# Kernel optimization log

Measured on AMD Instinct MI355X. Metric: run time of the kernel, lower is better.

Reference implementation:

```python
import jax, jax.numpy as jnp
import numpy as np

B, N, D, H = 4, 1024, 1024, 16
NP = N - 1  # prototypes; +1 CLS slot -> n_valid == N
HD = D // H
LN_EPS = 1e-5


def _build_spatial_sim(key):
    centers = jax.random.uniform(key, (NP, 2), dtype=jnp.float32) * 10.0
    diff = centers[:, None, :] - centers[None, :, :]
    d2 = jnp.sum(diff * diff, axis=-1)           # squared pairwise distance
    dist = jnp.sqrt(d2)
    sigma = dist.mean()                           # spatial_sigma = mean cdist
    sim = jnp.exp(-d2 / (2.0 * sigma * sigma))
    sim = sim / sim.max()
    ext = jnp.zeros((NP + 1, NP + 1), dtype=jnp.float32)
    ext = ext.at[0, :].set(1.0).at[:, 0].set(1.0).at[1:, 1:].set(sim)
    return ext


def setup_inputs() -> dict:
    key = jax.random.key(0)
    kc, kx, kq, kp = jax.random.split(key, 4)
    spatial_sim = _build_spatial_sim(kc)          # [N, N] buffer
    x = jax.random.normal(kx, (B, N, D), dtype=jnp.float32)
    gamma = jnp.ones((D,), dtype=jnp.float32)
    beta = jnp.zeros((D,), dtype=jnp.float32)
    w_qkv = jax.random.normal(kq, (D, 3 * D), dtype=jnp.float32) * 0.02
    w_proj = jax.random.normal(kp, (D, D), dtype=jnp.float32) * 0.02
    b_proj = jnp.zeros((D,), dtype=jnp.float32)
    swl = jnp.float32(np.log(0.3 / 0.7))          # inverse_sigmoid(0.3)
    return {"x": x, "gamma": gamma, "beta": beta, "w_qkv": w_qkv,
            "w_proj": w_proj, "b_proj": b_proj,
            "spatial_weight_logit": swl, "spatial_sim": spatial_sim}


def reference(x, gamma, beta, w_qkv, w_proj, b_proj, spatial_weight_logit, spatial_sim):
    b, n, d = x.shape
    scale = HD ** (-0.5)
    # LayerNorm (biased variance, eps=1e-5)
    mu = x.mean(axis=-1, keepdims=True)
    var = jnp.mean((x - mu) ** 2, axis=-1, keepdims=True)
    x_norm = (x - mu) / jnp.sqrt(var + LN_EPS) * gamma + beta
    # QKV projection -> [B, H, N, HD] each
    qkv = (x_norm @ w_qkv).reshape(b, n, 3, H, HD)
    qkv = jnp.transpose(qkv, (2, 0, 3, 1, 4))
    q, k, v = qkv[0], qkv[1], qkv[2]
    scores = jnp.einsum('bhnd,bhmd->bhnm', q, k) * scale
    alpha = jax.nn.sigmoid(spatial_weight_logit)
    # blend feature attention with fixed spatial similarity, then softmax
    attn = jax.nn.softmax((1.0 - alpha) * scores + alpha * spatial_sim[None, None], axis=-1)
    out = jnp.einsum('bhnm,bhmd->bhnd', attn, v)
    out = jnp.transpose(out, (0, 2, 1, 3)).reshape(b, n, d)
    out = out @ w_proj + b_proj
    return x + out
```

## Files before the change

### kernel.cpp

```cpp
#include <hip/hip_runtime.h>

#define Bz 4
#define Nn 1024
#define Dd 1024
#define Hh 16
#define HD 64
#define SCALE 0.125f
#define LN_EPS 1e-5f

typedef __attribute__((ext_vector_type(8))) __bf16 bf16x8;
typedef __attribute__((ext_vector_type(4))) float f32x4;

static __device__ inline unsigned short f2bf(float f) {
    unsigned int u = __float_as_uint(f);
    u += 0x7fffu + ((u >> 16) & 1u);
    return (unsigned short)(u >> 16);
}

static __device__ inline float bf2f(unsigned short s) {
    return __uint_as_float((unsigned)s << 16);
}

static __device__ inline bf16x8 ldfrag(const unsigned short* p) {
    return *(const bf16x8*)p;
}

static __device__ __forceinline__ void glds16(const unsigned short* g, unsigned short* l) {
    __builtin_amdgcn_global_load_lds((const __attribute__((address_space(1))) void*)g,
                                     (__attribute__((address_space(3))) void*)l, 16, 0, 0);
}

__global__ __launch_bounds__(256) void ln_kernel(const float* __restrict__ x,
                                                 const float* __restrict__ gamma,
                                                 const float* __restrict__ beta,
                                                 unsigned short* __restrict__ xn) {
    int row = blockIdx.x;
    int t = threadIdx.x;
    const float* xr = x + (size_t)row * Dd;
    float4 v = ((const float4*)xr)[t];
    float s = v.x + v.y + v.z + v.w;
    float ss = v.x * v.x + v.y * v.y + v.z * v.z + v.w * v.w;
    for (int o = 32; o > 0; o >>= 1) {
        s += __shfl_down(s, o);
        ss += __shfl_down(ss, o);
    }
    __shared__ float red[8];
    int wid = t >> 6;
    if ((t & 63) == 0) { red[wid * 2] = s; red[wid * 2 + 1] = ss; }
    __syncthreads();
    float tot = red[0] + red[2] + red[4] + red[6];
    float tot2 = red[1] + red[3] + red[5] + red[7];
    float mu = tot * (1.0f / Dd);
    float var = tot2 * (1.0f / Dd) - mu * mu;
    float inv = rsqrtf(var + LN_EPS);
    float4 g = ((const float4*)gamma)[t];
    float4 b = ((const float4*)beta)[t];
    ushort4 o4;
    o4.x = f2bf((v.x - mu) * inv * g.x + b.x);
    o4.y = f2bf((v.y - mu) * inv * g.y + b.y);
    o4.z = f2bf((v.z - mu) * inv * g.z + b.z);
    o4.w = f2bf((v.w - mu) * inv * g.w + b.w);
    ((ushort4*)(xn + (size_t)row * Dd))[t] = o4;
}

__global__ __launch_bounds__(256) void transpose_bf16(const float* __restrict__ in,
                                                      unsigned short* __restrict__ out,
                                                      int rows, int cols) {
    __shared__ float tile[32][33];
    int c0 = blockIdx.x * 32, r0 = blockIdx.y * 32;
    int tx = threadIdx.x, ty = threadIdx.y;
    for (int i = 0; i < 32; i += 8)
        tile[ty + i][tx] = in[(size_t)(r0 + ty + i) * cols + c0 + tx];
    __syncthreads();
    for (int i = 0; i < 32; i += 8)
        out[(size_t)(c0 + ty + i) * rows + r0 + tx] = f2bf(tile[tx][ty + i]);
}

__global__ __launch_bounds__(256) void conv_bf16(const float* __restrict__ in,
                                                 unsigned short* __restrict__ out) {
    int i = blockIdx.x * 256 + threadIdx.x;
    float4 v = ((const float4*)in)[i];
    ushort4 o;
    o.x = f2bf(v.x); o.y = f2bf(v.y); o.z = f2bf(v.z); o.w = f2bf(v.w);
    ((ushort4*)out)[i] = o;
}


__global__ __launch_bounds__(256) void gemm_qkv(const unsigned short* __restrict__ A,
                                                const unsigned short* __restrict__ Bt,
                                                unsigned short* __restrict__ qb,
                                                unsigned short* __restrict__ kb,
                                                unsigned short* __restrict__ vtb) {
    __shared__ unsigned short sA[8192], sB[8192];
    int tid = threadIdx.x;
    int w = tid >> 6, lane = tid & 63, lrow = lane & 15, quad = lane >> 4;
    int wm = w >> 1, wn = w & 1;
    int rowbase = blockIdx.y * 128;
    int colbase = blockIdx.x * 128;

    int srow = tid >> 3;
    int gch = ((tid & 7) - (srow >> 1)) & 7;
    const unsigned short* gA = A + (size_t)(rowbase + srow) * 1024 + gch * 8;
    const unsigned short* gB = Bt + (size_t)(colbase + srow) * 1024 + gch * 8;
    unsigned short* lA = sA + w * 512;
    unsigned short* lB = sB + w * 512;

    int bs0 = ((quad + (lrow >> 1)) & 7) * 8;
    int bs1 = ((4 + quad + (lrow >> 1)) & 7) * 8;
    const unsigned short* fa = sA + (wm * 64 + lrow) * 64;
    const unsigned short* fb = sB + (wn * 64 + lrow) * 64;

    f32x4 acc[4][4];
    #pragma unroll
    for (int i = 0; i < 4; i++)
        #pragma unroll
        for (int j = 0; j < 4; j++)
            acc[i][j] = (f32x4){0.f, 0.f, 0.f, 0.f};

    for (int k0 = 0; k0 < 1024; k0 += 64) {
        __syncthreads();
        #pragma unroll
        for (int c = 0; c < 4; c++) {
            glds16(gA + (size_t)c * 32768 + k0, lA + c * 2048);
            glds16(gB + (size_t)c * 32768 + k0, lB + c * 2048);
        }
        __syncthreads();
        #pragma unroll
        for (int s = 0; s < 2; s++) {
            int bo = s ? bs1 : bs0;
            bf16x8 a[4], b[4];
            #pragma unroll
            for (int i = 0; i < 4; i++) a[i] = *(const bf16x8*)(fa + i * 1024 + bo);
            #pragma unroll
            for (int j = 0; j < 4; j++) b[j] = *(const bf16x8*)(fb + j * 1024 + bo);
            #pragma unroll
            for (int i = 0; i < 4; i++)
                #pragma unroll
                for (int j = 0; j < 4; j++)
                    acc[i][j] = __builtin_amdgcn_mfma_f32_16x16x32_bf16(a[i], b[j], acc[i][j], 0, 0, 0);
        }
    }

    if (colbase < 2048) {
        #pragma unroll
        for (int j = 0; j < 4; j++) {
            int col = colbase + wn * 64 + j * 16 + lrow;
            int s = col >> 10, rem = col & 1023;
            int h = rem >> 6, e = rem & 63;
            unsigned short* dst = (s == 0) ? qb : kb;
            #pragma unroll
            for (int i = 0; i < 4; i++) {
                #pragma unroll
                for (int r = 0; r < 4; r++) {
                    int R = rowbase + wm * 64 + i * 16 + quad * 4 + r;
                    int bb = R >> 10, n = R & 1023;
                    dst[(((size_t)(bb * Hh + h)) * Nn + n) * HD + e] = f2bf(acc[i][j][r]);
                }
            }
        }
    } else {
        int bb = rowbase >> 10;
        int nbase = (rowbase & 1023) + wm * 64;
        unsigned short* sc = sA + w * 2048;
        int er = lane >> 2, nc = lane & 3;
        #pragma unroll
        for (int j = 0; j < 4; j++) {
            __syncthreads();
            int ebase = colbase + wn * 64 + j * 16 - 2048;
            int h = ebase >> 6, e0 = ebase & 63;
            #pragma unroll
            for (int i = 0; i < 4; i++) {
                uint2 pk;
                pk.x = (unsigned)f2bf(acc[i][j][0]) | ((unsigned)f2bf(acc[i][j][1]) << 16);
                pk.y = (unsigned)f2bf(acc[i][j][2]) | ((unsigned)f2bf(acc[i][j][3]) << 16);
                *(uint2*)(sc + lrow * 68 + i * 16 + quad * 4) = pk;
            }
            __syncthreads();
            unsigned short* vrow = vtb + ((size_t)((bb * Hh + h) * HD) + e0 + er) * Nn + nbase;
            #pragma unroll
            for (int c = 0; c < 4; c++) {
                uint2 v = *(const uint2*)(sc + er * 68 + c * 16 + nc * 4);
                *(uint2*)(vrow + c * 16 + nc * 4) = v;
            }
        }
    }
}

__global__ __launch_bounds__(256) void gemm_proj(const unsigned short* __restrict__ A,
                                                 const unsigned short* __restrict__ Bt,
                                                 const float* __restrict__ bias,
                                                 const float* __restrict__ x,
                                                 float* __restrict__ out) {
    __shared__ unsigned short sA[8192], sB[8192];
    int tid = threadIdx.x;
    int w = tid >> 6, lane = tid & 63, lrow = lane & 15, quad = lane >> 4;
    int wm = w >> 1, wn = w & 1;
    int rowbase = blockIdx.y * 128;
    int colbase = blockIdx.x * 128;

    int srow = tid >> 3;
    int gch = ((tid & 7) - (srow >> 1)) & 7;
    const unsigned short* gA = A + (size_t)(rowbase + srow) * 1024 + gch * 8;
    const unsigned short* gB = Bt + (size_t)(colbase + srow) * 1024 + gch * 8;
    unsigned short* lA = sA + w * 512;
    unsigned short* lB = sB + w * 512;

    int bs0 = ((quad + (lrow >> 1)) & 7) * 8;
    int bs1 = ((4 + quad + (lrow >> 1)) & 7) * 8;
    const unsigned short* fa = sA + (wm * 64 + lrow) * 64;
    const unsigned short* fb = sB + (wn * 64 + lrow) * 64;

    f32x4 acc[4][4];
    #pragma unroll
    for (int i = 0; i < 4; i++)
        #pragma unroll
        for (int j = 0; j < 4; j++)
            acc[i][j] = (f32x4){0.f, 0.f, 0.f, 0.f};

    for (int k0 = 0; k0 < 1024; k0 += 64) {
        __syncthreads();
        #pragma unroll
        for (int c = 0; c < 4; c++) {
            glds16(gA + (size_t)c * 32768 + k0, lA + c * 2048);
            glds16(gB + (size_t)c * 32768 + k0, lB + c * 2048);
        }
        __syncthreads();
        #pragma unroll
        for (int s = 0; s < 2; s++) {
            int bo = s ? bs1 : bs0;
            bf16x8 a[4], b[4];
            #pragma unroll
            for (int i = 0; i < 4; i++) a[i] = *(const bf16x8*)(fa + i * 1024 + bo);
            #pragma unroll
            for (int j = 0; j < 4; j++) b[j] = *(const bf16x8*)(fb + j * 1024 + bo);
            #pragma unroll
            for (int i = 0; i < 4; i++)
                #pragma unroll
                for (int j = 0; j < 4; j++)
                    acc[i][j] = __builtin_amdgcn_mfma_f32_16x16x32_bf16(a[i], b[j], acc[i][j], 0, 0, 0);
        }
    }

    #pragma unroll
    for (int j = 0; j < 4; j++) {
        int col = colbase + wn * 64 + j * 16 + lrow;
        float bc = bias[col];
        #pragma unroll
        for (int i = 0; i < 4; i++) {
            #pragma unroll
            for (int r = 0; r < 4; r++) {
                int R = rowbase + wm * 64 + i * 16 + quad * 4 + r;
                out[(size_t)R * 1024 + col] = acc[i][j][r] + bc + x[(size_t)R * 1024 + col];
            }
        }
    }
}

#define PSTR 72
__global__ __launch_bounds__(256) void attn_kernel(const unsigned short* __restrict__ qb,
                                                   const unsigned short* __restrict__ kb,
                                                   const unsigned short* __restrict__ vtb,
                                                   const unsigned short* __restrict__ simb,
                                                   const float* __restrict__ swl,
                                                   unsigned short* __restrict__ aout) {
    int h = blockIdx.y, bb = blockIdx.z;
    int n0 = blockIdx.x * 128;
    int tid = threadIdx.x;
    int w = tid >> 6, lane = tid & 63;
    int lrow = lane & 15, quad = lane >> 4;
    const unsigned short* q = qb + ((size_t)(bb * Hh + h)) * Nn * HD;
    const unsigned short* k = kb + ((size_t)(bb * Hh + h)) * Nn * HD;
    const unsigned short* vt = vtb + ((size_t)(bb * Hh + h)) * HD * Nn;
    float alpha = 1.f / (1.f + __expf(-swl[0]));
    float c1 = (1.f - alpha) * SCALE;

    __shared__ unsigned short sK[4096];
    __shared__ unsigned short sV[4096];
    __shared__ unsigned short sP[128 * PSTR];

    int qr0 = n0 + w * 32;
    bf16x8 qf[2][2];
    #pragma unroll
    for (int g = 0; g < 2; g++) {
        qf[g][0] = ldfrag(q + (size_t)(qr0 + g * 16 + lrow) * HD + quad * 8);
        qf[g][1] = ldfrag(q + (size_t)(qr0 + g * 16 + lrow) * HD + 32 + quad * 8);
    }

    f32x4 o[2][4];
    #pragma unroll
    for (int g = 0; g < 2; g++)
        #pragma unroll
        for (int et = 0; et < 4; et++) o[g][et] = (f32x4){0.f, 0.f, 0.f, 0.f};
    float rsum[2] = {0.f, 0.f};

    int bs0 = (quad + (lrow >> 1)) & 7;
    int bs1 = (4 + quad + (lrow >> 1)) & 7;
    unsigned short* sPw = sP + (w * 32) * PSTR;

    for (int m0 = 0; m0 < 1024; m0 += 64) {
        __syncthreads();
        #pragma unroll
        for (int i = 0; i < 2; i++) {
            int slot = i * 256 + tid;
            int row = slot >> 3;
            int cg = ((slot & 7) - (row >> 1)) & 7;
            glds16(k + (size_t)(m0 + row) * HD + cg * 8, sK + i * 2048 + w * 512);
        }
        #pragma unroll
        for (int i = 0; i < 2; i++) {
            int slot = i * 256 + tid;
            int row = slot >> 3;
            int cg = ((slot & 7) - (row >> 1)) & 7;
            glds16(vt + (size_t)row * Nn + m0 + cg * 8, sV + i * 2048 + w * 512);
        }
        ushort4 sm[4][2];
        #pragma unroll
        for (int ks = 0; ks < 4; ks++)
            #pragma unroll
            for (int g = 0; g < 2; g++)
                sm[ks][g] = *(const ushort4*)(simb + (size_t)(qr0 + g * 16 + lrow) * Nn
                                              + m0 + ks * 16 + quad * 4);
        __syncthreads();

        #pragma unroll
        for (int ks = 0; ks < 4; ks++) {
            const unsigned short* kr = sK + (ks * 16 + lrow) * 64;
            bf16x8 ak0 = *(const bf16x8*)(kr + bs0 * 8);
            bf16x8 ak1 = *(const bf16x8*)(kr + bs1 * 8);
            #pragma unroll
            for (int g = 0; g < 2; g++) {
                f32x4 c = (f32x4){0.f, 0.f, 0.f, 0.f};
                c = __builtin_amdgcn_mfma_f32_16x16x32_bf16(ak0, qf[g][0], c, 0, 0, 0);
                c = __builtin_amdgcn_mfma_f32_16x16x32_bf16(ak1, qf[g][1], c, 0, 0, 0);
                const unsigned short* smp = (const unsigned short*)&sm[ks][g];
                float e0 = __expf(c1 * c[0] + alpha * bf2f(smp[0]));
                float e1 = __expf(c1 * c[1] + alpha * bf2f(smp[1]));
                float e2 = __expf(c1 * c[2] + alpha * bf2f(smp[2]));
                float e3 = __expf(c1 * c[3] + alpha * bf2f(smp[3]));
                rsum[g] += (e0 + e1) + (e2 + e3);
                uint2 pk;
                pk.x = (__float_as_uint(e0) >> 16) | (__float_as_uint(e1) & 0xffff0000u);
                pk.y = (__float_as_uint(e2) >> 16) | (__float_as_uint(e3) & 0xffff0000u);
                *(uint2*)(sPw + (g * 16 + lrow) * PSTR + ks * 16 + quad * 4) = pk;
            }
        }

        #pragma unroll
        for (int ms = 0; ms < 2; ms++) {
            bf16x8 pa[2];
            #pragma unroll
            for (int g = 0; g < 2; g++)
                pa[g] = *(const bf16x8*)(sPw + (g * 16 + lrow) * PSTR + ms * 32 + quad * 8);
            #pragma unroll
            for (int et = 0; et < 4; et++) {
                int e = et * 16 + lrow;
                int slot = (ms * 4 + quad + (e >> 1)) & 7;
                bf16x8 vb = *(const bf16x8*)(sV + e * 64 + slot * 8);
                #pragma unroll
                for (int g = 0; g < 2; g++)
                    o[g][et] = __builtin_amdgcn_mfma_f32_16x16x32_bf16(pa[g], vb, o[g][et], 0, 0, 0);
            }
        }
    }

    #pragma unroll
    for (int g = 0; g < 2; g++) {
        rsum[g] += __shfl_xor(rsum[g], 16);
        rsum[g] += __shfl_xor(rsum[g], 32);
    }

    #pragma unroll
    for (int g = 0; g < 2; g++)
        #pragma unroll
        for (int r = 0; r < 4; r++) {
            float inv = 1.f / __shfl(rsum[g], quad * 4 + r);
            int qn = qr0 + g * 16 + quad * 4 + r;
            #pragma unroll
            for (int et = 0; et < 4; et++)
                aout[((size_t)bb * Nn + qn) * Dd + h * HD + et * 16 + lrow]
                    = f2bf(o[g][et][r] * inv);
        }
}

extern "C" void kernel_launch(void* const* d_in, const int* in_sizes, int n_in,
                              void* d_out, int out_size, void* d_ws, size_t ws_size,
                              hipStream_t stream) {
    const float* x      = (const float*)d_in[0];
    const float* gamma  = (const float*)d_in[1];
    const float* beta   = (const float*)d_in[2];
    const float* w_qkv  = (const float*)d_in[3];
    const float* w_proj = (const float*)d_in[4];
    const float* b_proj = (const float*)d_in[5];
    const float* swl    = (const float*)d_in[6];
    const float* sim    = (const float*)d_in[7];
    float* out = (float*)d_out;

    unsigned short* ws = (unsigned short*)d_ws;
    unsigned short* xn     = ws;
    unsigned short* wqkvT  = xn + 4194304;
    unsigned short* wprojT = wqkvT + 3145728;
    unsigned short* qb     = wprojT + 1048576;
    unsigned short* kb     = qb + 4194304;
    unsigned short* vtb    = kb + 4194304;
    unsigned short* aout   = vtb + 4194304;
    unsigned short* simb   = xn;

    transpose_bf16<<<dim3(3072 / 32, 1024 / 32), dim3(32, 8), 0, stream>>>(w_qkv, wqkvT, 1024, 3072);
    transpose_bf16<<<dim3(1024 / 32, 1024 / 32), dim3(32, 8), 0, stream>>>(w_proj, wprojT, 1024, 1024);
    ln_kernel<<<4096, 256, 0, stream>>>(x, gamma, beta, xn);
    gemm_qkv<<<dim3(24, 32), 256, 0, stream>>>(xn, wqkvT, qb, kb, vtb);
    conv_bf16<<<1024, 256, 0, stream>>>(sim, simb);
    attn_kernel<<<dim3(8, 16, 4), 256, 0, stream>>>(qb, kb, vtb, simb, swl, aout);
    gemm_proj<<<dim3(8, 32), 256, 0, stream>>>(aout, wprojT, b_proj, x, out);
}
```

Baseline: 206.0 us.

## Merge LayerNorm and weight transposes into one prep kernel; read fp32 sim directly

LayerNorm and both weight transpose-to-bf16 passes now run as a single launch, with block index ranges selecting the work, which saves two kernel launches. The separate conversion of the spatial similarity matrix to bf16 is removed, and the attention kernel loads the fp32 similarity values directly. This drops one launch and one full pass over the matrix, but the attention kernel now reads twice as many bytes of similarity per tile, 1024x1024 floats reused across all batch and head blocks and likely held in cache.

```diff
diff --git a/kernel.cpp b/kernel.cpp
--- a/kernel.cpp
+++ b/kernel.cpp
@@ -17,10 +17,6 @@
     return (unsigned short)(u >> 16);
 }
 
-static __device__ inline float bf2f(unsigned short s) {
-    return __uint_as_float((unsigned)s << 16);
-}
-
 static __device__ inline bf16x8 ldfrag(const unsigned short* p) {
     return *(const bf16x8*)p;
 }
@@ -30,59 +26,66 @@
                                      (__attribute__((address_space(3))) void*)l, 16, 0, 0);
 }
 
-__global__ __launch_bounds__(256) void ln_kernel(const float* __restrict__ x,
-                                                 const float* __restrict__ gamma,
-                                                 const float* __restrict__ beta,
-                                                 unsigned short* __restrict__ xn) {
-    int row = blockIdx.x;
-    int t = threadIdx.x;
-    const float* xr = x + (size_t)row * Dd;
-    float4 v = ((const float4*)xr)[t];
-    float s = v.x + v.y + v.z + v.w;
-    float ss = v.x * v.x + v.y * v.y + v.z * v.z + v.w * v.w;
-    for (int o = 32; o > 0; o >>= 1) {
-        s += __shfl_down(s, o);
-        ss += __shfl_down(ss, o);
-    }
-    __shared__ float red[8];
-    int wid = t >> 6;
-    if ((t & 63) == 0) { red[wid * 2] = s; red[wid * 2 + 1] = ss; }
-    __syncthreads();
-    float tot = red[0] + red[2] + red[4] + red[6];
-    float tot2 = red[1] + red[3] + red[5] + red[7];
-    float mu = tot * (1.0f / Dd);
-    float var = tot2 * (1.0f / Dd) - mu * mu;
-    float inv = rsqrtf(var + LN_EPS);
-    float4 g = ((const float4*)gamma)[t];
-    float4 b = ((const float4*)beta)[t];
-    ushort4 o4;
-    o4.x = f2bf((v.x - mu) * inv * g.x + b.x);
-    o4.y = f2bf((v.y - mu) * inv * g.y + b.y);
-    o4.z = f2bf((v.z - mu) * inv * g.z + b.z);
-    o4.w = f2bf((v.w - mu) * inv * g.w + b.w);
-    ((ushort4*)(xn + (size_t)row * Dd))[t] = o4;
-}
-
-__global__ __launch_bounds__(256) void transpose_bf16(const float* __restrict__ in,
-                                                      unsigned short* __restrict__ out,
-                                                      int rows, int cols) {
+__global__ __launch_bounds__(256) void prep_kernel(const float* __restrict__ x,
+                                                   const float* __restrict__ gamma,
+                                                   const float* __restrict__ beta,
+                                                   unsigned short* __restrict__ xn,
+                                                   const float* __restrict__ w_qkv,
+                                                   unsigned short* __restrict__ wqkvT,
+                                                   const float* __restrict__ w_proj,
+                                                   unsigned short* __restrict__ wprojT) {
     __shared__ float tile[32][33];
-    int c0 = blockIdx.x * 32, r0 = blockIdx.y * 32;
-    int tx = threadIdx.x, ty = threadIdx.y;
-    for (int i = 0; i < 32; i += 8)
-        tile[ty + i][tx] = in[(size_t)(r0 + ty + i) * cols + c0 + tx];
-    __syncthreads();
-    for (int i = 0; i < 32; i += 8)
-        out[(size_t)(c0 + ty + i) * rows + r0 + tx] = f2bf(tile[tx][ty + i]);
-}
-
-__global__ __launch_bounds__(256) void conv_bf16(const float* __restrict__ in,
-                                                 unsigned short* __restrict__ out) {
-    int i = blockIdx.x * 256 + threadIdx.x;
-    float4 v = ((const float4*)in)[i];
-    ushort4 o;
-    o.x = f2bf(v.x); o.y = f2bf(v.y); o.z = f2bf(v.z); o.w = f2bf(v.w);
-    ((ushort4*)out)[i] = o;
+    int blk = blockIdx.x;
+    int tid = threadIdx.x;
+
+    if (blk < 4096) {
+        const float* xr = x + (size_t)blk * Dd;
+        float4 v = ((const float4*)xr)[tid];
+        float s = v.x + v.y + v.z + v.w;
+        float ss = v.x * v.x + v.y * v.y + v.z * v.z + v.w * v.w;
+        for (int o = 32; o > 0; o >>= 1) {
+            s += __shfl_down(s, o);
+            ss += __shfl_down(ss, o);
+        }
+        float* red = &tile[0][0];
+        int wid = tid >> 6;
+        if ((tid & 63) == 0) { red[wid * 2] = s; red[wid * 2 + 1] = ss; }
+        __syncthreads();
+        float tot = red[0] + red[2] + red[4] + red[6];
+        float tot2 = red[1] + red[3] + red[5] + red[7];
+        float mu = tot * (1.0f / Dd);
+        float var = tot2 * (1.0f / Dd) - mu * mu;
+        float inv = rsqrtf(var + LN_EPS);
+        float4 g = ((const float4*)gamma)[tid];
+        float4 b = ((const float4*)beta)[tid];
+        ushort4 o4;
+        o4.x = f2bf((v.x - mu) * inv * g.x + b.x);
+        o4.y = f2bf((v.y - mu) * inv * g.y + b.y);
+        o4.z = f2bf((v.z - mu) * inv * g.z + b.z);
+        o4.w = f2bf((v.w - mu) * inv * g.w + b.w);
+        ((ushort4*)(xn + (size_t)blk * Dd))[tid] = o4;
+    } else {
+        const float* in;
+        unsigned short* out;
+        int cols, c0, r0;
+        if (blk < 7168) {
+            int idx = blk - 4096;
+            in = w_qkv; out = wqkvT; cols = 3072;
+            c0 = (idx % 96) * 32; r0 = (idx / 96) * 32;
+        } else {
+            int idx = blk - 7168;
+            in = w_proj; out = wprojT; cols = 1024;
+            c0 = (idx % 32) * 32; r0 = (idx / 32) * 32;
+        }
+        int tx = tid & 31, ty = tid >> 5;
+        #pragma unroll
+        for (int i = 0; i < 32; i += 8)
+            tile[ty + i][tx] = in[(size_t)(r0 + ty + i) * cols + c0 + tx];
+        __syncthreads();
+        #pragma unroll
+        for (int i = 0; i < 32; i += 8)
+            out[(size_t)(c0 + ty + i) * 1024 + r0 + tx] = f2bf(tile[tx][ty + i]);
+    }
 }
 
 
@@ -260,7 +263,7 @@
 __global__ __launch_bounds__(256) void attn_kernel(const unsigned short* __restrict__ qb,
                                                    const unsigned short* __restrict__ kb,
                                                    const unsigned short* __restrict__ vtb,
-                                                   const unsigned short* __restrict__ simb,
+                                                   const float* __restrict__ sim,
                                                    const float* __restrict__ swl,
                                                    unsigned short* __restrict__ aout) {
     int h = blockIdx.y, bb = blockIdx.z;
@@ -313,13 +316,13 @@
             int cg = ((slot & 7) - (row >> 1)) & 7;
             glds16(vt + (size_t)row * Nn + m0 + cg * 8, sV + i * 2048 + w * 512);
         }
-        ushort4 sm[4][2];
+        float4 sm[4][2];
         #pragma unroll
         for (int ks = 0; ks < 4; ks++)
             #pragma unroll
             for (int g = 0; g < 2; g++)
-                sm[ks][g] = *(const ushort4*)(simb + (size_t)(qr0 + g * 16 + lrow) * Nn
-                                              + m0 + ks * 16 + quad * 4);
+                sm[ks][g] = *(const float4*)(sim + (size_t)(qr0 + g * 16 + lrow) * Nn
+                                             + m0 + ks * 16 + quad * 4);
         __syncthreads();
 
         #pragma unroll
@@ -332,11 +335,10 @@
                 f32x4 c = (f32x4){0.f, 0.f, 0.f, 0.f};
                 c = __builtin_amdgcn_mfma_f32_16x16x32_bf16(ak0, qf[g][0], c, 0, 0, 0);
                 c = __builtin_amdgcn_mfma_f32_16x16x32_bf16(ak1, qf[g][1], c, 0, 0, 0);
-                const unsigned short* smp = (const unsigned short*)&sm[ks][g];
-                float e0 = __expf(c1 * c[0] + alpha * bf2f(smp[0]));
-                float e1 = __expf(c1 * c[1] + alpha * bf2f(smp[1]));
-                float e2 = __expf(c1 * c[2] + alpha * bf2f(smp[2]));
-                float e3 = __expf(c1 * c[3] + alpha * bf2f(smp[3]));
+                float e0 = __expf(c1 * c[0] + alpha * sm[ks][g].x);
+                float e1 = __expf(c1 * c[1] + alpha * sm[ks][g].y);
+                float e2 = __expf(c1 * c[2] + alpha * sm[ks][g].z);
+                float e3 = __expf(c1 * c[3] + alpha * sm[ks][g].w);
                 rsum[g] += (e0 + e1) + (e2 + e3);
                 uint2 pk;
                 pk.x = (__float_as_uint(e0) >> 16) | (__float_as_uint(e1) & 0xffff0000u);
@@ -403,13 +405,9 @@
     unsigned short* kb     = qb + 4194304;
     unsigned short* vtb    = kb + 4194304;
     unsigned short* aout   = vtb + 4194304;
-    unsigned short* simb   = xn;
-
-    transpose_bf16<<<dim3(3072 / 32, 1024 / 32), dim3(32, 8), 0, stream>>>(w_qkv, wqkvT, 1024, 3072);
-    transpose_bf16<<<dim3(1024 / 32, 1024 / 32), dim3(32, 8), 0, stream>>>(w_proj, wprojT, 1024, 1024);
-    ln_kernel<<<4096, 256, 0, stream>>>(x, gamma, beta, xn);
+
+    prep_kernel<<<8192, 256, 0, stream>>>(x, gamma, beta, xn, w_qkv, wqkvT, w_proj, wprojT);
     gemm_qkv<<<dim3(24, 32), 256, 0, stream>>>(xn, wqkvT, qb, kb, vtb);
-    conv_bf16<<<1024, 256, 0, stream>>>(sim, simb);
-    attn_kernel<<<dim3(8, 16, 4), 256, 0, stream>>>(qb, kb, vtb, simb, swl, aout);
+    attn_kernel<<<dim3(8, 16, 4), 256, 0, stream>>>(qb, kb, vtb, sim, swl, aout);
     gemm_proj<<<dim3(8, 32), 256, 0, stream>>>(aout, wprojT, b_proj, x, out);
 }
```

Measured after the change: 199.4 us. -3.2%, faster.
